# Kernel tuning notes

Measured on AMD Instinct MI355X. Metric: run time of the kernel, lower is better.

## Reference

```python
import jax, jax.numpy as jnp
import numpy as np

N_EMBD = 1024
N_HEAD = 16
HEAD_DIM = N_EMBD / N_HEAD  # used only for the attention scale, as in the source
LN_EPS = 1e-5


def _layernorm(x, g, b):
    mu = jnp.mean(x, axis=-1, keepdims=True)
    var = jnp.mean(jnp.square(x - mu), axis=-1, keepdims=True)
    return (x - mu) * jax.lax.rsqrt(var + LN_EPS) * g + b


def setup_inputs() -> dict:
    key = jax.random.key(0)
    ks = jax.random.split(key, 8)
    D = N_EMBD
    s = lambda n: 0.02  # GPT-style init scale
    x = jax.random.normal(ks[0], (4, 2048, D), dtype=jnp.float32)
    w_attn = jax.random.normal(ks[1], (D, 3 * D), dtype=jnp.float32) * s(D)
    b_attn = jnp.zeros((3 * D,), jnp.float32)
    w_proj = jax.random.normal(ks[2], (D, D), dtype=jnp.float32) * s(D)
    b_proj = jnp.zeros((D,), jnp.float32)
    ln1_g = jnp.ones((D,), jnp.float32)
    ln1_b = jnp.zeros((D,), jnp.float32)
    ln2_g = jnp.ones((D,), jnp.float32)
    ln2_b = jnp.zeros((D,), jnp.float32)
    w_fc = jax.random.normal(ks[3], (D, 4 * D), dtype=jnp.float32) * s(D)
    b_fc = jnp.zeros((4 * D,), jnp.float32)
    w_fc2 = jax.random.normal(ks[4], (4 * D, D), dtype=jnp.float32) * s(4 * D)
    b_fc2 = jnp.zeros((D,), jnp.float32)
    return {"x": x, "w_attn": w_attn, "b_attn": b_attn, "w_proj": w_proj,
            "b_proj": b_proj, "ln1_g": ln1_g, "ln1_b": ln1_b, "ln2_g": ln2_g,
            "ln2_b": ln2_b, "w_fc": w_fc, "b_fc": b_fc, "w_fc2": w_fc2,
            "b_fc2": b_fc2}


def reference(x, w_attn, b_attn, w_proj, b_proj, ln1_g, ln1_b, ln2_g, ln2_b,
              w_fc, b_fc, w_fc2, b_fc2):
    B, T, D = x.shape
    # --- attention branch (pre-LN) ---
    h = _layernorm(x, ln1_g, ln1_b)
    qkv = h @ w_attn + b_attn                     # [B,T,3D]
    q, k, v = jnp.split(qkv, 3, axis=-1)
    scale = 1.0 / np.sqrt(HEAD_DIM).astype(np.float32)
    att = jnp.einsum('btd,bsd->bts', q, k) * scale  # full-dim scores [B,T,T]
    causal = jnp.tril(jnp.ones((T, T), dtype=bool))
    att = jnp.where(causal[None, :, :], att, -jnp.inf)
    att = jax.nn.softmax(att, axis=-1)
    y = jnp.einsum('bts,bsd->btd', att, v)
    y = y @ w_proj + b_proj
    x = x + y
    # --- MLP branch (pre-LN) ---
    h = _layernorm(x, ln2_g, ln2_b)
    h = jax.nn.gelu(h @ w_fc + b_fc, approximate=True)
    h = h @ w_fc2 + b_fc2
    return x + h
```

## Files before the change

### kernel.cpp

```cpp
#include <hip/hip_runtime.h>
#include <math.h>


typedef unsigned short u16;
typedef __attribute__((ext_vector_type(8))) short bf16x8;
typedef __attribute__((ext_vector_type(8))) unsigned short u16x8;
typedef __attribute__((ext_vector_type(4))) float f32x4;

#define DEV __device__ __forceinline__

#define GLOAD_LDS16(gp, lp)                                                     \
    __builtin_amdgcn_global_load_lds(                                           \
        (const __attribute__((address_space(1))) void*)(gp),                    \
        (__attribute__((address_space(3))) void*)(lp), 16, 0, 0)

#define DSR128(dst_, p_)                                                        \
    asm volatile("ds_read_b128 %0, %1"                                          \
                 : "=v"(dst_)                                                   \
                 : "v"((unsigned)(unsigned long long)                           \
                       (__attribute__((address_space(3))) const void*)(p_)))

DEV float bf2f(u16 h) {
    union { unsigned u; float f; } t; t.u = ((unsigned)h) << 16; return t.f;
}
DEV u16 f2bf(float f) {
    union { unsigned u; float f; } t; t.f = f;
    unsigned u = t.u;
    return (u16)((u + 0x7FFFu + ((u >> 16) & 1u)) >> 16);
}
DEV float loadIn(const void* p, long i, int isbf) {
    return isbf ? bf2f(((const u16*)p)[i]) : ((const float*)p)[i];
}
DEV float gelu_fast(float x) {
    float u = 1.5957691216057308f * (x + 0.044715f * x * x * x);
    return x * __builtin_amdgcn_rcpf(1.0f + __expf(-u));
}

DEV float waveSum(float v) {
    #pragma unroll
    for (int o = 32; o > 0; o >>= 1) v += __shfl_down(v, o, 64);
    return v;
}
DEV float waveMax(float v) {
    #pragma unroll
    for (int o = 32; o > 0; o >>= 1) v = fmaxf(v, __shfl_down(v, o, 64));
    return v;
}

template <bool IS_MAX>
DEV float blockReduce(float v) {
    __shared__ float tmp[5];
    __syncthreads();
    v = IS_MAX ? waveMax(v) : waveSum(v);
    int lane = threadIdx.x & 63, w = threadIdx.x >> 6;
    if (lane == 0) tmp[w] = v;
    __syncthreads();
    if (threadIdx.x == 0) {
        float r = tmp[0];
        for (int i = 1; i < 4; i++) r = IS_MAX ? fmaxf(r, tmp[i]) : (r + tmp[i]);
        tmp[4] = r;
    }
    __syncthreads();
    return tmp[4];
}

__global__ void detect_dtype(const u16* __restrict__ xr, int* __restrict__ flag) {
    const int tid = threadIdx.x;
    int cnt = 0;
    #pragma unroll
    for (int i = 0; i < 16; i++) {
        unsigned u = xr[2 * (tid + 256 * i)];
        unsigned e = (u >> 7) & 0xFF;
        cnt += (e >= 100 && e <= 140) ? 1 : 0;
    }
    __shared__ int sh[4];
    #pragma unroll
    for (int o = 32; o > 0; o >>= 1) cnt += __shfl_down(cnt, o, 64);
    if ((tid & 63) == 0) sh[tid >> 6] = cnt;
    __syncthreads();
    if (tid == 0) flag[0] = (sh[0] + sh[1] + sh[2] + sh[3] > 2048) ? 1 : 0;
}

template <bool RAW_IN>
__global__ void ln_kernel(const void* __restrict__ x, const void* __restrict__ g,
                          const void* __restrict__ b, u16* __restrict__ out,
                          const int* __restrict__ flagp) {
    const int isbf = *flagp;
    const int inbf = RAW_IN ? isbf : 1;
    const long base = (long)blockIdx.x * 1024;
    const int tid = threadIdx.x;
    float v[4];
    #pragma unroll
    for (int j = 0; j < 4; j++) v[j] = loadIn(x, base + tid + 256 * j, inbf);
    float mu = blockReduce<false>(v[0] + v[1] + v[2] + v[3]) * (1.0f / 1024.0f);
    float d[4], sq = 0.f;
    #pragma unroll
    for (int j = 0; j < 4; j++) { d[j] = v[j] - mu; sq += d[j] * d[j]; }
    float var = blockReduce<false>(sq) * (1.0f / 1024.0f);
    float rstd = rsqrtf(var + 1e-5f);
    #pragma unroll
    for (int j = 0; j < 4; j++) {
        int c = tid + 256 * j;
        out[base + c] = f2bf(d[j] * rstd * loadIn(g, c, isbf) + loadIn(b, c, isbf));
    }
}

__global__ void transpose_to_bf16(const void* __restrict__ in, int ldin, long inBatch,
                                  u16* __restrict__ out, int ldout, long outBatch,
                                  const int* __restrict__ flagp) {
    __shared__ u16 tile[32][33];
    const int isbf = flagp ? *flagp : 1;
    const long ibase = (long)blockIdx.z * inBatch;
    out += (long)blockIdx.z * outBatch;
    const int bc = blockIdx.x * 32, br = blockIdx.y * 32;
    const int tx = threadIdx.x & 31, ty = threadIdx.x >> 5;
    #pragma unroll
    for (int i = 0; i < 32; i += 8)
        tile[ty + i][tx] = f2bf(loadIn(in, ibase + (long)(br + ty + i) * ldin + bc + tx, isbf));
    __syncthreads();
    #pragma unroll
    for (int i = 0; i < 32; i += 8)
        out[(long)(bc + ty + i) * ldout + br + tx] = tile[tx][ty + i];
}

template <int MODE, int CAUSAL>
__global__ __launch_bounds__(512, 2) void gemm_8ph(
        const u16* __restrict__ A, int lda, long aBatch,
        const u16* __restrict__ Bt, int ldb, long bBatch,
        const void* __restrict__ bias,
        void* __restrict__ Cv, int ldc, long cBatch,
        const void* __restrict__ res,
        float scale, const int* __restrict__ flagp, int K) {
    __shared__ __align__(16) u16 sA[2][256 * 64];
    __shared__ __align__(16) u16 sB[2][256 * 64];

    int m0, n0;
    if (CAUSAL == 1) {
        const int bx = blockIdx.x;
        int ti = (int)((sqrtf(8.0f * bx + 1.0f) - 1.0f) * 0.5f);
        while ((ti + 1) * (ti + 2) / 2 <= bx) ++ti;
        while (ti * (ti + 1) / 2 > bx) --ti;
        m0 = ti * 256;
        n0 = (bx - ti * (ti + 1) / 2) * 256;
    } else if (CAUSAL == 2) {
        m0 = blockIdx.y * 256;
        n0 = blockIdx.x * 256;
    } else {
        const int gx  = gridDim.x;
        const int nwg = gx * gridDim.y;
        const int fid = blockIdx.y * gx + blockIdx.x;
        const int swz = (fid & 7) * (nwg >> 3) + (fid >> 3);
        m0 = (swz / gx) * 256;
        n0 = (swz % gx) * 256;
    }
    const int bz = blockIdx.z;
    A  += (long)bz * aBatch;
    Bt += (long)bz * bBatch;

    const int tid  = threadIdx.x;
    const int lane = tid & 63, wv = tid >> 6;
    const int wm = wv >> 2, wn = wv & 3;
    const int l16 = lane & 15, quad = lane >> 4;
    const int xg = l16 & 7;

    const int rq   = tid >> 3;
    const int gsrc = ((tid & 7) ^ (rq & 7)) * 8;
    const int gdst = (tid & 7) * 8;
    const int rAb  = (rq < 32) ? rq : 96 + rq;

    int NT = K >> 6;
    if (CAUSAL == 2) NT = min(K, m0 + 256) >> 6;

#define STAGE8(t_, q_) do {                                                      \
        const int sl_ = (t_) & 1;                                                \
        const int k0_ = (t_) << 6;                                               \
        const int ra_ = ((q_) << 5) + rAb;                                       \
        GLOAD_LDS16(A + (long)(m0 + ra_) * lda + k0_ + gsrc,                     \
                    &sA[sl_][ra_ * 64 + gdst]);                                  \
        const int rb_ = ((q_) << 6) + rq;                                        \
        GLOAD_LDS16(Bt + (long)(n0 + rb_) * ldb + k0_ + gsrc,                    \
                    &sB[sl_][rb_ * 64 + gdst]);                                  \
    } while (0)

#define PBAR8() do { __builtin_amdgcn_sched_barrier(0);                          \
        asm volatile("s_barrier" ::: "memory");                                  \
        __builtin_amdgcn_sched_barrier(0); } while (0)

#define WVM8(n_) do { __builtin_amdgcn_sched_barrier(0);                         \
        asm volatile("s_waitcnt vmcnt(" #n_ ")" ::: "memory");                   \
        __builtin_amdgcn_sched_barrier(0); } while (0)

#define WLGKM(n_) do { __builtin_amdgcn_sched_barrier(0);                        \
        asm volatile("s_waitcnt lgkmcnt(" #n_ ")" ::: "memory");                 \
        __builtin_amdgcn_sched_barrier(0); } while (0)

#define RD_A(buf_, qn_, sl_) do {                                                \
        DSR128(buf_[0][0], &sA[sl_][(wm * 128 + (2 * (qn_) + 0) * 16 + l16) * 64 \
                                    + (((0 * 4 + quad) ^ xg) * 8)]);             \
        DSR128(buf_[0][1], &sA[sl_][(wm * 128 + (2 * (qn_) + 0) * 16 + l16) * 64 \
                                    + (((1 * 4 + quad) ^ xg) * 8)]);             \
        DSR128(buf_[1][0], &sA[sl_][(wm * 128 + (2 * (qn_) + 1) * 16 + l16) * 64 \
                                    + (((0 * 4 + quad) ^ xg) * 8)]);             \
        DSR128(buf_[1][1], &sA[sl_][(wm * 128 + (2 * (qn_) + 1) * 16 + l16) * 64 \
                                    + (((1 * 4 + quad) ^ xg) * 8)]);             \
    } while (0)

#define RD_B(sl_) do {                                                           \
        DSR128(bC[0][0], &sB[sl_][(wn * 64 + 0 * 16 + l16) * 64 + (((0 * 4 + quad) ^ xg) * 8)]); \
        DSR128(bC[0][1], &sB[sl_][(wn * 64 + 0 * 16 + l16) * 64 + (((1 * 4 + quad) ^ xg) * 8)]); \
        DSR128(bC[1][0], &sB[sl_][(wn * 64 + 1 * 16 + l16) * 64 + (((0 * 4 + quad) ^ xg) * 8)]); \
        DSR128(bC[1][1], &sB[sl_][(wn * 64 + 1 * 16 + l16) * 64 + (((1 * 4 + quad) ^ xg) * 8)]); \
        DSR128(bC[2][0], &sB[sl_][(wn * 64 + 2 * 16 + l16) * 64 + (((0 * 4 + quad) ^ xg) * 8)]); \
        DSR128(bC[2][1], &sB[sl_][(wn * 64 + 2 * 16 + l16) * 64 + (((1 * 4 + quad) ^ xg) * 8)]); \
        DSR128(bC[3][0], &sB[sl_][(wn * 64 + 3 * 16 + l16) * 64 + (((0 * 4 + quad) ^ xg) * 8)]); \
        DSR128(bC[3][1], &sB[sl_][(wn * 64 + 3 * 16 + l16) * 64 + (((1 * 4 + quad) ^ xg) * 8)]); \
    } while (0)

#define MFMA_PH(q_, A_) do {                                                     \
        __builtin_amdgcn_s_setprio(1);                                           \
        _Pragma("unroll")                                                        \
        for (int f_ = 0; f_ < 2; ++f_)                                           \
            _Pragma("unroll")                                                    \
            for (int j_ = 0; j_ < 4; ++j_) {                                     \
                acc[2 * (q_) + f_][j_] = __builtin_amdgcn_mfma_f32_16x16x32_bf16(\
                    A_[f_][0], bC[j_][0], acc[2 * (q_) + f_][j_], 0, 0, 0);      \
                acc[2 * (q_) + f_][j_] = __builtin_amdgcn_mfma_f32_16x16x32_bf16(\
                    A_[f_][1], bC[j_][1], acc[2 * (q_) + f_][j_], 0, 0, 0);      \
            }                                                                    \
        __builtin_amdgcn_s_setprio(0);                                           \
    } while (0)

    f32x4 acc[8][4];
    #pragma unroll
    for (int i = 0; i < 8; i++)
        #pragma unroll
        for (int j = 0; j < 4; j++) acc[i][j] = f32x4{0.f, 0.f, 0.f, 0.f};

    bf16x8 afA[2][2], afB[2][2], bC[4][2];

    STAGE8(0, 0); STAGE8(0, 1); STAGE8(0, 2); STAGE8(0, 3);
    STAGE8(1, 0); STAGE8(1, 1); STAGE8(1, 2);
    WVM8(6);
    PBAR8();
    RD_A(afA, 0, 0);

    for (int u = 0; u < NT; ++u) {
        const int su = u & 1, sn = su ^ 1;
        if (u + 1 < NT) STAGE8(u + 1, 3);
        __builtin_amdgcn_sched_barrier(0);
        RD_B(su);
        RD_A(afB, 1, su);
        WLGKM(4);
        MFMA_PH(0, afA);
        PBAR8();
        if (u + 2 < NT) STAGE8(u + 2, 0);
        __builtin_amdgcn_sched_barrier(0);
        RD_A(afA, 2, su);
        WLGKM(4);
        MFMA_PH(1, afB);
        PBAR8();
        if (u + 2 < NT) STAGE8(u + 2, 1);
        __builtin_amdgcn_sched_barrier(0);
        RD_A(afB, 3, su);
        WLGKM(4);
        MFMA_PH(2, afA);
        PBAR8();
        if (u + 2 < NT) { STAGE8(u + 2, 2); WVM8(6); } else { WVM8(0); }
        PBAR8();
        RD_A(afA, 0, sn);
        WLGKM(4);
        MFMA_PH(3, afB);
        PBAR8();
    }
    WLGKM(0);

    const int isbf = (MODE == 0 || MODE == 3 || MODE == 4 || MODE == 5) ? *flagp : 1;
    #pragma unroll
    for (int mi = 0; mi < 8; ++mi) {
        #pragma unroll
        for (int j = 0; j < 4; ++j) {
            #pragma unroll
            for (int r = 0; r < 4; ++r) {
                const int row = m0 + wm * 128 + mi * 16 + quad * 4 + r;
                const int col = n0 + wn * 64 + j * 16 + l16;
                const long idx = (long)bz * cBatch + (long)row * ldc + col;
                float v = acc[mi][j][r];
                if (MODE == 1) {
                    reinterpret_cast<u16*>(Cv)[idx] = f2bf(v * scale);
                } else if (MODE == 2) {
                    reinterpret_cast<u16*>(Cv)[idx] = f2bf(v);
                } else {
                    v += loadIn(bias, col, isbf);
                    if (MODE == 4) v = gelu_fast(v);
                    if (MODE == 3) v += loadIn(res, (long)row * ldc + col, isbf);
                    if (MODE == 5) v += bf2f(((const u16*)res)[(long)row * ldc + col]);
                    if (MODE == 5 && !isbf)
                        reinterpret_cast<float*>(Cv)[idx] = v;
                    else
                        reinterpret_cast<u16*>(Cv)[idx] = f2bf(v);
                }
            }
        }
    }
#undef STAGE8
#undef PBAR8
#undef WVM8
#undef WLGKM
#undef RD_A
#undef RD_B
#undef MFMA_PH
}

__global__ void softmax_causal(const u16* __restrict__ S, u16* __restrict__ P) {
    const long row = blockIdx.x;
    const int t = (int)(row & 2047);
    const u16* sr = S + row * 2048;
    u16* pr = P + row * 2048;
    const int tid = threadIdx.x;
    const int s0 = tid * 8;
    float v[8];
    float mx = -INFINITY;
    if (s0 <= t) {
        u16x8 raw = *reinterpret_cast<const u16x8*>(sr + s0);
        #pragma unroll
        for (int i = 0; i < 8; i++) {
            float x = bf2f(raw[i]);
            v[i] = (s0 + i <= t) ? x : -INFINITY;
            mx = fmaxf(mx, v[i]);
        }
    } else {
        #pragma unroll
        for (int i = 0; i < 8; i++) v[i] = -INFINITY;
    }
    mx = blockReduce<true>(mx);
    float sum = 0.f;
    #pragma unroll
    for (int i = 0; i < 8; i++) {
        float e = (v[i] == -INFINITY) ? 0.0f : __expf(v[i] - mx);
        v[i] = e;
        sum += e;
    }
    sum = blockReduce<false>(sum);
    float inv = 1.0f / sum;
    if (s0 <= (t | 255)) {
        u16x8 o;
        #pragma unroll
        for (int i = 0; i < 8; i++) o[i] = f2bf(v[i] * inv);
        *reinterpret_cast<u16x8*>(pr + s0) = o;
    }
}

extern "C" void kernel_launch(void* const* d_in, const int* in_sizes, int n_in,
                              void* d_out, int out_size, void* d_ws, size_t ws_size,
                              hipStream_t stream) {
    const void* x      = d_in[0];
    const void* w_attn = d_in[1];
    const void* b_attn = d_in[2];
    const void* w_proj = d_in[3];
    const void* b_proj = d_in[4];
    const void* ln1_g  = d_in[5];
    const void* ln1_b  = d_in[6];
    const void* ln2_g  = d_in[7];
    const void* ln2_b  = d_in[8];
    const void* w_fc   = d_in[9];
    const void* b_fc   = d_in[10];
    const void* w_fc2  = d_in[11];
    const void* b_fc2  = d_in[12];

    char* ws = (char*)d_ws;
    u16*   hbuf   = (u16*)(ws);
    u16*   qkv    = (u16*)(ws + 16777216);
    u16*   S      = (u16*)(ws + 67108864);
    u16*   wattnT = (u16*)(ws + 134217728);
    u16*   wprojT = wattnT + 3072 * 1024;
    u16*   wfcT   = wprojT + 1024 * 1024;
    u16*   wfc2T  = wfcT + 4096 * 1024;
    u16*   vT     = wfc2T + 1024 * 4096;
    int*   flag   = (int*)(ws + 176160768);
    u16*   probs  = qkv;
    u16*   x1     = qkv + 16777216;

    detect_dtype<<<1, 256, 0, stream>>>((const u16*)x, flag);

    transpose_to_bf16<<<dim3(96, 32, 1),  256, 0, stream>>>(w_attn, 3072, 0, wattnT, 1024, 0, flag);
    transpose_to_bf16<<<dim3(32, 32, 1),  256, 0, stream>>>(w_proj, 1024, 0, wprojT, 1024, 0, flag);
    transpose_to_bf16<<<dim3(128, 32, 1), 256, 0, stream>>>(w_fc,   4096, 0, wfcT,   1024, 0, flag);
    transpose_to_bf16<<<dim3(32, 128, 1), 256, 0, stream>>>(w_fc2,  1024, 0, wfc2T,  4096, 0, flag);

    ln_kernel<true><<<8192, 256, 0, stream>>>(x, ln1_g, ln1_b, hbuf, flag);

    gemm_8ph<0, 0><<<dim3(12, 32, 1), 512, 0, stream>>>(
        hbuf, 1024, 0, wattnT, 1024, 0, b_attn, qkv, 3072, 0, nullptr, 0.f, flag, 1024);

    transpose_to_bf16<<<dim3(32, 64, 4), 256, 0, stream>>>(
        qkv + 2048, 3072, (long)2048 * 3072, vT, 2048, (long)1024 * 2048, nullptr);

    gemm_8ph<1, 1><<<dim3(36, 1, 4), 512, 0, stream>>>(
        qkv, 3072, (long)2048 * 3072, qkv + 1024, 3072, (long)2048 * 3072,
        nullptr, S, 2048, (long)2048 * 2048, nullptr, 0.125f, flag, 1024);

    softmax_causal<<<8192, 256, 0, stream>>>(S, probs);

    gemm_8ph<2, 2><<<dim3(4, 8, 4), 512, 0, stream>>>(
        probs, 2048, (long)2048 * 2048, vT, 2048, (long)1024 * 2048,
        nullptr, hbuf, 1024, (long)2048 * 1024, nullptr, 0.f, flag, 2048);

    gemm_8ph<3, 0><<<dim3(4, 32, 1), 512, 0, stream>>>(
        hbuf, 1024, 0, wprojT, 1024, 0, b_proj, x1, 1024, 0, x, 0.f, flag, 1024);

    ln_kernel<false><<<8192, 256, 0, stream>>>(x1, ln2_g, ln2_b, hbuf, flag);

    gemm_8ph<4, 0><<<dim3(16, 32, 1), 512, 0, stream>>>(
        hbuf, 1024, 0, wfcT, 1024, 0, b_fc, S, 4096, 0, nullptr, 0.f, flag, 1024);

    gemm_8ph<5, 0><<<dim3(4, 32, 1), 512, 0, stream>>>(
        S, 4096, 0, wfc2T, 4096, 0, b_fc2, d_out, 1024, 0, x1, 0.f, flag, 4096);
}
```

Baseline: 686.5 us.

## Restructure GEMM main loop into full-tile prefetch with split B fragment reads

Replaces the quarter-tile staged pipeline, which had barriers between each MFMA phase, with a loop that issues the whole next K-tile's global-to-LDS loads at the top of the iteration. It then interleaves half-width A and B fragment LDS reads with MFMA groups and synchronizes once at the end. This removes the per-phase barriers and the setprio hints and shortens register live ranges for B fragments. The cost is that it waits for all outstanding global loads (vmcnt 0) every iteration, so load latency overlaps with only one tile of compute. It also reverses the row-block order for the CAUSAL==2 grid so blocks with longer K ranges launch first.

Result: faster. 665.8 us (-3.0%).

```diff
diff --git a/kernel.cpp b/kernel.cpp
--- a/kernel.cpp
+++ b/kernel.cpp
@@ -143,7 +143,7 @@
         m0 = ti * 256;
         n0 = (bx - ti * (ti + 1) / 2) * 256;
     } else if (CAUSAL == 2) {
-        m0 = blockIdx.y * 256;
+        m0 = (gridDim.y - 1 - blockIdx.y) * 256;
         n0 = blockIdx.x * 256;
     } else {
         const int gx  = gridDim.x;
@@ -182,19 +182,17 @@
                     &sB[sl_][rb_ * 64 + gdst]);                                  \
     } while (0)
 
-#define PBAR8() do { __builtin_amdgcn_sched_barrier(0);                          \
-        asm volatile("s_barrier" ::: "memory");                                  \
-        __builtin_amdgcn_sched_barrier(0); } while (0)
-
-#define WVM8(n_) do { __builtin_amdgcn_sched_barrier(0);                         \
+#define BAR8() asm volatile("s_barrier" ::: "memory")
+
+#define WVMC(n_) do {                                                            \
         asm volatile("s_waitcnt vmcnt(" #n_ ")" ::: "memory");                   \
         __builtin_amdgcn_sched_barrier(0); } while (0)
 
-#define WLGKM(n_) do { __builtin_amdgcn_sched_barrier(0);                        \
+#define WLGKM(n_) do {                                                           \
         asm volatile("s_waitcnt lgkmcnt(" #n_ ")" ::: "memory");                 \
         __builtin_amdgcn_sched_barrier(0); } while (0)
 
-#define RD_A(buf_, qn_, sl_) do {                                                \
+#define RD_A4(buf_, qn_, sl_) do {                                               \
         DSR128(buf_[0][0], &sA[sl_][(wm * 128 + (2 * (qn_) + 0) * 16 + l16) * 64 \
                                     + (((0 * 4 + quad) ^ xg) * 8)]);             \
         DSR128(buf_[0][1], &sA[sl_][(wm * 128 + (2 * (qn_) + 0) * 16 + l16) * 64 \
@@ -205,29 +203,31 @@
                                     + (((1 * 4 + quad) ^ xg) * 8)]);             \
     } while (0)
 
-#define RD_B(sl_) do {                                                           \
-        DSR128(bC[0][0], &sB[sl_][(wn * 64 + 0 * 16 + l16) * 64 + (((0 * 4 + quad) ^ xg) * 8)]); \
-        DSR128(bC[0][1], &sB[sl_][(wn * 64 + 0 * 16 + l16) * 64 + (((1 * 4 + quad) ^ xg) * 8)]); \
-        DSR128(bC[1][0], &sB[sl_][(wn * 64 + 1 * 16 + l16) * 64 + (((0 * 4 + quad) ^ xg) * 8)]); \
-        DSR128(bC[1][1], &sB[sl_][(wn * 64 + 1 * 16 + l16) * 64 + (((1 * 4 + quad) ^ xg) * 8)]); \
-        DSR128(bC[2][0], &sB[sl_][(wn * 64 + 2 * 16 + l16) * 64 + (((0 * 4 + quad) ^ xg) * 8)]); \
-        DSR128(bC[2][1], &sB[sl_][(wn * 64 + 2 * 16 + l16) * 64 + (((1 * 4 + quad) ^ xg) * 8)]); \
-        DSR128(bC[3][0], &sB[sl_][(wn * 64 + 3 * 16 + l16) * 64 + (((0 * 4 + quad) ^ xg) * 8)]); \
-        DSR128(bC[3][1], &sB[sl_][(wn * 64 + 3 * 16 + l16) * 64 + (((1 * 4 + quad) ^ xg) * 8)]); \
+#define RD_B4(buf_, jp_, sl_) do {                                               \
+        DSR128(buf_[0][0], &sB[sl_][(wn * 64 + (2 * (jp_) + 0) * 16 + l16) * 64  \
+                                    + (((0 * 4 + quad) ^ xg) * 8)]);             \
+        DSR128(buf_[0][1], &sB[sl_][(wn * 64 + (2 * (jp_) + 0) * 16 + l16) * 64  \
+                                    + (((1 * 4 + quad) ^ xg) * 8)]);             \
+        DSR128(buf_[1][0], &sB[sl_][(wn * 64 + (2 * (jp_) + 1) * 16 + l16) * 64  \
+                                    + (((0 * 4 + quad) ^ xg) * 8)]);             \
+        DSR128(buf_[1][1], &sB[sl_][(wn * 64 + (2 * (jp_) + 1) * 16 + l16) * 64  \
+                                    + (((1 * 4 + quad) ^ xg) * 8)]);             \
     } while (0)
 
-#define MFMA_PH(q_, A_) do {                                                     \
-        __builtin_amdgcn_s_setprio(1);                                           \
+#define MFMA8(mq_, jp_, A_, B_) do {                                             \
         _Pragma("unroll")                                                        \
         for (int f_ = 0; f_ < 2; ++f_)                                           \
             _Pragma("unroll")                                                    \
-            for (int j_ = 0; j_ < 4; ++j_) {                                     \
-                acc[2 * (q_) + f_][j_] = __builtin_amdgcn_mfma_f32_16x16x32_bf16(\
-                    A_[f_][0], bC[j_][0], acc[2 * (q_) + f_][j_], 0, 0, 0);      \
-                acc[2 * (q_) + f_][j_] = __builtin_amdgcn_mfma_f32_16x16x32_bf16(\
-                    A_[f_][1], bC[j_][1], acc[2 * (q_) + f_][j_], 0, 0, 0);      \
+            for (int jj_ = 0; jj_ < 2; ++jj_) {                                  \
+                acc[2 * (mq_) + f_][2 * (jp_) + jj_] =                           \
+                    __builtin_amdgcn_mfma_f32_16x16x32_bf16(                     \
+                        A_[f_][0], B_[jj_][0],                                   \
+                        acc[2 * (mq_) + f_][2 * (jp_) + jj_], 0, 0, 0);          \
+                acc[2 * (mq_) + f_][2 * (jp_) + jj_] =                           \
+                    __builtin_amdgcn_mfma_f32_16x16x32_bf16(                     \
+                        A_[f_][1], B_[jj_][1],                                   \
+                        acc[2 * (mq_) + f_][2 * (jp_) + jj_], 0, 0, 0);          \
             }                                                                    \
-        __builtin_amdgcn_s_setprio(0);                                           \
     } while (0)
 
     f32x4 acc[8][4];
@@ -236,41 +236,37 @@
         #pragma unroll
         for (int j = 0; j < 4; j++) acc[i][j] = f32x4{0.f, 0.f, 0.f, 0.f};
 
-    bf16x8 afA[2][2], afB[2][2], bC[4][2];
+    bf16x8 afA[2][2], afB[2][2], bJ0[2][2], bJ1[2][2];
 
     STAGE8(0, 0); STAGE8(0, 1); STAGE8(0, 2); STAGE8(0, 3);
-    STAGE8(1, 0); STAGE8(1, 1); STAGE8(1, 2);
-    WVM8(6);
-    PBAR8();
-    RD_A(afA, 0, 0);
+    WVMC(0);
+    BAR8();
+    RD_A4(afA, 0, 0);
+    RD_B4(bJ0, 0, 0);
 
     for (int u = 0; u < NT; ++u) {
         const int su = u & 1, sn = su ^ 1;
-        if (u + 1 < NT) STAGE8(u + 1, 3);
-        __builtin_amdgcn_sched_barrier(0);
-        RD_B(su);
-        RD_A(afB, 1, su);
-        WLGKM(4);
-        MFMA_PH(0, afA);
-        PBAR8();
-        if (u + 2 < NT) STAGE8(u + 2, 0);
-        __builtin_amdgcn_sched_barrier(0);
-        RD_A(afA, 2, su);
-        WLGKM(4);
-        MFMA_PH(1, afB);
-        PBAR8();
-        if (u + 2 < NT) STAGE8(u + 2, 1);
-        __builtin_amdgcn_sched_barrier(0);
-        RD_A(afB, 3, su);
-        WLGKM(4);
-        MFMA_PH(2, afA);
-        PBAR8();
-        if (u + 2 < NT) { STAGE8(u + 2, 2); WVM8(6); } else { WVM8(0); }
-        PBAR8();
-        RD_A(afA, 0, sn);
-        WLGKM(4);
-        MFMA_PH(3, afB);
-        PBAR8();
+        if (u + 1 < NT) { STAGE8(u + 1, 0); STAGE8(u + 1, 1);
+                          STAGE8(u + 1, 2); STAGE8(u + 1, 3); }
+        RD_B4(bJ1, 1, su);
+        WLGKM(4); MFMA8(0, 0, afA, bJ0);
+        RD_A4(afB, 1, su);
+        WLGKM(4); MFMA8(0, 1, afA, bJ1);
+        WLGKM(0); MFMA8(1, 1, afB, bJ1);
+        RD_A4(afA, 2, su);
+        WLGKM(4); MFMA8(1, 0, afB, bJ0);
+        WLGKM(0); MFMA8(2, 0, afA, bJ0);
+        RD_A4(afB, 3, su);
+        WLGKM(4); MFMA8(2, 1, afA, bJ1);
+        WLGKM(0); MFMA8(3, 1, afB, bJ1);
+        MFMA8(3, 0, afB, bJ0);
+        BAR8();
+        WVMC(0);
+        BAR8();
+        if (u + 1 < NT) {
+            RD_A4(afA, 0, sn);
+            RD_B4(bJ0, 0, sn);
+        }
     }
     WLGKM(0);
 
@@ -303,12 +299,12 @@
         }
     }
 #undef STAGE8
-#undef PBAR8
-#undef WVM8
+#undef BAR8
+#undef WVMC
 #undef WLGKM
-#undef RD_A
-#undef RD_B
-#undef MFMA_PH
+#undef RD_A4
+#undef RD_B4
+#undef MFMA8
 }
 
 __global__ void softmax_causal(const u16* __restrict__ S, u16* __restrict__ P) {
```
